# Optimization experiments

Measured on AMD Instinct MI355X. Metric: run time of the kernel, lower is better.

Reference implementation:

```python
import jax, jax.numpy as jnp
import numpy as np
import math

N_HEADS = 16
HEAD_DIM = 64
ROPE_BASE = 10000.0


def _rope_tables(T, head_dim, dtype):
    inv_freq = 1.0 / (ROPE_BASE ** (jnp.arange(0, head_dim, 2, dtype=jnp.float32) / head_dim))
    t = jnp.arange(T, dtype=jnp.float32)
    freqs = jnp.outer(t, inv_freq)          # (T, head_dim/2)
    emb = jnp.concatenate([freqs, freqs], axis=-1)  # (T, head_dim)
    return jnp.cos(emb).astype(dtype), jnp.sin(emb).astype(dtype)


def _rotate_half(x):
    x1, x2 = jnp.split(x, 2, axis=-1)
    return jnp.concatenate([-x2, x1], axis=-1)


def setup_inputs() -> dict:
    key = jax.random.key(0)
    k1, k2, k3 = jax.random.split(key, 3)
    B, T, D = 2, 2048, 1024
    x = jax.random.normal(k1, (B, T, D), dtype=jnp.float32)
    W_qkv = jax.random.normal(k2, (D, 3 * D), dtype=jnp.float32) * (1.0 / math.sqrt(D))
    W_proj = jax.random.normal(k3, (D, D), dtype=jnp.float32) * (1.0 / math.sqrt(D))
    return {"x": x, "W_qkv": W_qkv, "W_proj": W_proj}


def reference(x, W_qkv, W_proj):
    B, T, C = x.shape
    H, Dh = N_HEADS, HEAD_DIM
    qkv = x @ W_qkv                                   # (B,T,3C)
    q, k, v = jnp.split(qkv, 3, axis=-1)
    # (B,T,C) -> (B,H,T,Dh)
    q = q.reshape(B, T, H, Dh).transpose(0, 2, 1, 3)
    k = k.reshape(B, T, H, Dh).transpose(0, 2, 1, 3)
    v = v.reshape(B, T, H, Dh).transpose(0, 2, 1, 3)
    cos, sin = _rope_tables(T, Dh, x.dtype)           # (T,Dh)
    q = q * cos + _rotate_half(q) * sin
    k = k * cos + _rotate_half(k) * sin
    scale = 1.0 / math.sqrt(Dh)
    att = jnp.einsum('bhqd,bhkd->bhqk', q, k) * scale
    causal = jnp.tril(jnp.ones((T, T), dtype=bool))
    att = jnp.where(causal, att, -jnp.inf)
    att = jax.nn.softmax(att, axis=-1)
    y = jnp.einsum('bhqk,bhkd->bhqd', att, v)         # (B,H,T,Dh)
    y = y.transpose(0, 2, 1, 3).reshape(B, T, C)
    return y @ W_proj
```

## Files before the change

kernel.cpp:

```cpp
#include <hip/hip_runtime.h>
#include <hip/hip_bf16.h>
#include <math.h>

typedef __bf16 bf16_t;
typedef __bf16 bf16x8 __attribute__((ext_vector_type(8)));
typedef __bf16 bf16x4 __attribute__((ext_vector_type(4)));
typedef __bf16 bf16x2 __attribute__((ext_vector_type(2)));
typedef float  f32x4  __attribute__((ext_vector_type(4)));
typedef float  f32x16 __attribute__((ext_vector_type(16)));

__device__ __forceinline__ void gload_lds16(const void* g, void* l) {
  __builtin_amdgcn_global_load_lds((const __attribute__((address_space(1))) void*)g,
                                   (__attribute__((address_space(3))) void*)l,
                                   16, 0, 0);
}

__device__ __forceinline__ unsigned pk2(float a, float b) {
  union { bf16x2 h; unsigned u; } x;
  x.h[0] = (bf16_t)a; x.h[1] = (bf16_t)b;
  return x.u;
}
__device__ __forceinline__ bf16x8 frag4(unsigned w0, unsigned w1, unsigned w2, unsigned w3) {
  union { unsigned u[4]; bf16x8 f; } x;
  x.u[0] = w0; x.u[1] = w1; x.u[2] = w2; x.u[3] = w3;
  return x.f;
}
__device__ __forceinline__ void pls(unsigned a, unsigned b, unsigned& x, unsigned& y) {
  auto rr = __builtin_amdgcn_permlane32_swap(a, b, false, false);
  x = ((unsigned*)&rr)[0];
  y = ((unsigned*)&rr)[1];
}

__global__ __launch_bounds__(256) void f32_to_bf16(const float* __restrict__ x,
                                                   bf16_t* __restrict__ y, int n) {
  int i = blockIdx.x * blockDim.x + threadIdx.x;
  int idx = i * 4;
  if (idx < n) {
    float4 v = *(const float4*)(x + idx);
    bf16x4 o;
    o[0] = (bf16_t)v.x; o[1] = (bf16_t)v.y; o[2] = (bf16_t)v.z; o[3] = (bf16_t)v.w;
    *(bf16x4*)(y + idx) = o;
  }
}

__global__ __launch_bounds__(256) void transpose_w(const float* __restrict__ W,
                                                   bf16_t* __restrict__ Wt,
                                                   int K, int N) {
  __shared__ float tile[32][33];
  int tx = threadIdx.x & 31, ty = threadIdx.x >> 5;
  int n0 = blockIdx.x * 32, k0 = blockIdx.y * 32;
  #pragma unroll
  for (int i = 0; i < 4; ++i) {
    int k = ty + i * 8;
    tile[k][tx] = W[(size_t)(k0 + k) * N + n0 + tx];
  }
  __syncthreads();
  #pragma unroll
  for (int i = 0; i < 4; ++i) {
    int r = ty + i * 8;
    Wt[(size_t)(n0 + r) * K + k0 + tx] = (bf16_t)tile[tx][r];
  }
}

__global__ void rope_tables(float* __restrict__ cosT, float* __restrict__ sinT) {
  int t = blockIdx.x, d = threadIdx.x;
  float inv = __expf(-logf(10000.f) * (float)(d & 31) * (1.f / 32.f));
  float ang = (float)t * inv;
  cosT[t * 64 + d] = cosf(ang);
  sinT[t * 64 + d] = sinf(ang);
}

template <int OUT_BF16>
__global__ __launch_bounds__(256) void gemm_bt(const bf16_t* __restrict__ A,
                                               const bf16_t* __restrict__ Bt,
                                               void* __restrict__ Cout,
                                               int M, int N, int K) {
  const int tid = threadIdx.x;
  const int l = tid & 63, w = tid >> 6;
  const int lr = l & 15, lg = l >> 4;
  const int nwgx = gridDim.x, nwgy = gridDim.y;
  const int orig = blockIdx.y * nwgx + blockIdx.x;
  const int cpx = (nwgx * nwgy) >> 3;
  const int s_id = (orig & 7) * cpx + (orig >> 3);
  const int bx = s_id / nwgy;
  const int by = s_id % nwgy;
  const int wr = w >> 1, wc = w & 1;
  __shared__ __align__(16) bf16_t lA[128 * 64];
  __shared__ __align__(16) bf16_t lB[128 * 64];
  f32x4 acc[4][4];
  const f32x4 zf = {0.f, 0.f, 0.f, 0.f};
  #pragma unroll
  for (int m = 0; m < 4; ++m)
    #pragma unroll
    for (int n = 0; n < 4; ++n) acc[m][n] = zf;

  const int sr8 = l >> 3;
  const int sc16 = ((l & 7) * 16) ^ (sr8 << 4);
  const char* Ab = (const char*)(A + (size_t)(by * 128) * K);
  const char* Bb = (const char*)(Bt + (size_t)(bx * 128) * K);
  const size_t rowb = (size_t)K * 2;

  for (int k0 = 0; k0 < 2 * K; k0 += 128) {
    #pragma unroll
    for (int p = 0; p < 4; ++p) {
      int row = p * 32 + w * 8 + sr8;
      gload_lds16(Ab + (size_t)row * rowb + k0 + sc16, (char*)lA + p * 4096 + w * 1024);
      gload_lds16(Bb + (size_t)row * rowb + k0 + sc16, (char*)lB + p * 4096 + w * 1024);
    }
    __syncthreads();
    #pragma unroll
    for (int kk = 0; kk < 2; ++kk) {
      bf16x8 aF[4], bF[4];
      #pragma unroll
      for (int m = 0; m < 4; ++m) {
        int row = wr * 64 + m * 16 + lr;
        aF[m] = *(const bf16x8*)((const char*)lA + row * 128 +
                                 ((kk * 64 + lg * 16) ^ ((row & 7) << 4)));
      }
      #pragma unroll
      for (int n = 0; n < 4; ++n) {
        int row = wc * 64 + n * 16 + lr;
        bF[n] = *(const bf16x8*)((const char*)lB + row * 128 +
                                 ((kk * 64 + lg * 16) ^ ((row & 7) << 4)));
      }
      __builtin_amdgcn_s_setprio(1);
      #pragma unroll
      for (int m = 0; m < 4; ++m)
        #pragma unroll
        for (int n = 0; n < 4; ++n)
          acc[m][n] = __builtin_amdgcn_mfma_f32_16x16x32_bf16(aF[m], bF[n], acc[m][n], 0, 0, 0);
      __builtin_amdgcn_s_setprio(0);
    }
    __syncthreads();
  }

  const int orow0 = by * 128 + wr * 64;
  const int ocol0 = bx * 128 + wc * 64;
  if (OUT_BF16) {
    bf16_t* C = (bf16_t*)Cout;
    #pragma unroll
    for (int m = 0; m < 4; ++m)
      #pragma unroll
      for (int n = 0; n < 4; ++n)
        #pragma unroll
        for (int r = 0; r < 4; ++r)
          C[(size_t)(orow0 + m * 16 + lg * 4 + r) * N + ocol0 + n * 16 + lr] =
              (bf16_t)acc[m][n][r];
  } else {
    float* C = (float*)Cout;
    #pragma unroll
    for (int m = 0; m < 4; ++m)
      #pragma unroll
      for (int n = 0; n < 4; ++n)
        #pragma unroll
        for (int r = 0; r < 4; ++r)
          C[(size_t)(orow0 + m * 16 + lg * 4 + r) * N + ocol0 + n * 16 + lr] =
              acc[m][n][r];
  }
}

__global__ __launch_bounds__(256) void prep_qk(const bf16_t* __restrict__ qkv,
                                               const float* __restrict__ cosT,
                                               const float* __restrict__ sinT,
                                               bf16_t* __restrict__ Q,
                                               bf16_t* __restrict__ Kr) {
  int gid = blockIdx.x * 4 + (threadIdx.x >> 6);
  int d = threadIdx.x & 63;
  int t = gid & 2047, bh = gid >> 11;
  int b = bh >> 4, h = bh & 15;
  const bf16_t* row = qkv + (size_t)(b * 2048 + t) * 3072 + h * 64;
  float q = (float)row[d];
  float k = (float)row[1024 + d];
  float c = cosT[t * 64 + d], s = sinT[t * 64 + d];
  float qp = __shfl_xor(q, 32);
  float kp = __shfl_xor(k, 32);
  float qr = (d < 32) ? -qp : qp;
  float krot = (d < 32) ? -kp : kp;
  size_t o = ((size_t)bh * 2048 + t) * 64 + d;
  Q[o] = (bf16_t)((q * c + qr * s) * 0.18033688011112042f);
  Kr[o] = (bf16_t)(k * c + krot * s);
}

__global__ __launch_bounds__(256) void prep_vt(const bf16_t* __restrict__ qkv,
                                               bf16_t* __restrict__ VT) {
  int bh = blockIdx.x, b = bh >> 4, h = bh & 15;
  int t0 = blockIdx.y * 64;
  __shared__ __align__(16) bf16_t tile[64][72];
  int r = threadIdx.x >> 2, c4 = threadIdx.x & 3;
  const bf16_t* src = qkv + (size_t)(b * 2048 + t0 + r) * 3072 + 2048 + h * 64 + c4 * 16;
  *(bf16x8*)&tile[r][c4 * 16] = *(const bf16x8*)src;
  *(bf16x8*)&tile[r][c4 * 16 + 8] = *(const bf16x8*)(src + 8);
  __syncthreads();
  bf16x8 v0, v1;
  #pragma unroll
  for (int i = 0; i < 8; ++i) v0[i] = tile[c4 * 16 + i][r];
  #pragma unroll
  for (int i = 0; i < 8; ++i) v1[i] = tile[c4 * 16 + 8 + i][r];
  bf16_t* dst = VT + ((size_t)bh * 64 + r) * 2048 + t0 + c4 * 16;
  *(bf16x8*)dst = v0;
  *(bf16x8*)(dst + 8) = v1;
}

__global__ __launch_bounds__(512, 4) void attn(const bf16_t* __restrict__ Q,
                                               const bf16_t* __restrict__ K,
                                               const bf16_t* __restrict__ VT,
                                               bf16_t* __restrict__ Y) {
  const int L = blockIdx.x;
  const int bh = L & 31;
  const int idx = (L & 255) >> 5;
  const int qi = (L >= 256) ? (15 - 2 * idx) : (2 * idx);
  const int b = bh >> 4, h = bh & 15;
  const int tid = threadIdx.x, l = tid & 63, w = tid >> 6;
  const int qw = w & 3, half = w >> 2;
  const int tid2 = tid & 255;
  const int l31 = l & 31, hi = l >> 5;
  const int hi4 = hi * 4, hi8 = hi * 8;
  const int qbase = qi * 128 + qw * 32;
  const int qown = qbase + l31;
  const int ntile = qi + 1;
  const int t0 = half * ntile, tend = t0 + ntile;
  const int tdiag = qbase >> 6;

  __shared__ __align__(16) char smem[65536];
  char* Kbase = smem + half * 16384;
  char* Vbase = smem + 32768 + half * 16384;

  const bf16_t* Qb = Q + (size_t)bh * 2048 * 64;
  const bf16_t* Kb0 = K + (size_t)bh * 2048 * 64;
  const bf16_t* Vb = VT + (size_t)bh * 64 * 2048;

  bf16x8 qf[4];
  #pragma unroll
  for (int kk = 0; kk < 4; ++kk)
    qf[kk] = *(const bf16x8*)(Qb + (size_t)qown * 64 + kk * 16 + hi8);

  const int srow = tid2 >> 3;
  const int scolb = (tid2 & 7) * 16;
  const int rA = srow, rB = 32 + srow;
  const int swA = scolb ^ ((rA & 7) << 4);
  const int swB = scolb ^ ((rB & 7) << 4);
  const char* KgA = (const char*)Kb0 + (size_t)t0 * 8192 + (size_t)rA * 128 + swA;
  const char* KgB = (const char*)Kb0 + (size_t)t0 * 8192 + (size_t)rB * 128 + swB;
  const char* VgA = (const char*)Vb + (size_t)t0 * 128 + (size_t)rA * 4096 + swA;
  const char* VgB = (const char*)Vb + (size_t)t0 * 128 + (size_t)rB * 4096 + swB;

  f32x16 oa[2];
  #pragma unroll
  for (int dt = 0; dt < 2; ++dt)
    #pragma unroll
    for (int r = 0; r < 16; ++r) oa[dt][r] = 0.f;
  float lacc0 = 0.f, lacc1 = 0.f;

  gload_lds16(KgA, Kbase + tid2 * 16);
  gload_lds16(KgB, Kbase + 4096 + tid2 * 16);
  gload_lds16(VgA, Vbase + tid2 * 16);
  gload_lds16(VgB, Vbase + 4096 + tid2 * 16);
  KgA += 8192; KgB += 8192; VgA += 128; VgB += 128;
  __syncthreads();

  int cur = 0;
  for (int t = t0; t < tend; ++t) {
    if (t + 1 < tend) {
      char* dK = Kbase + (cur ^ 1) * 8192;
      char* dV = Vbase + (cur ^ 1) * 8192;
      gload_lds16(KgA, dK + tid2 * 16);
      gload_lds16(KgB, dK + 4096 + tid2 * 16);
      gload_lds16(VgA, dV + tid2 * 16);
      gload_lds16(VgB, dV + 4096 + tid2 * 16);
      KgA += 8192; KgB += 8192; VgA += 128; VgB += 128;
    }
    const char* KlH = Kbase + cur * 8192;
    const char* VlH = Vbase + cur * 8192;

    if (t <= tdiag) {
      f32x16 s[2];
      #pragma unroll
      for (int sb = 0; sb < 2; ++sb)
        #pragma unroll
        for (int r = 0; r < 16; ++r) s[sb][r] = 0.f;
      __builtin_amdgcn_s_setprio(1);
      #pragma unroll
      for (int sb = 0; sb < 2; ++sb) {
        int row = sb * 32 + l31;
        const char* kr = KlH + row * 128;
        int sw = (row & 7) << 4;
        #pragma unroll
        for (int kk = 0; kk < 4; ++kk) {
          bf16x8 kf = *(const bf16x8*)(kr + ((kk * 32 + hi * 16) ^ sw));
          s[sb] = __builtin_amdgcn_mfma_f32_32x32x16_bf16(kf, qf[kk], s[sb], 0, 0, 0);
        }
      }
      __builtin_amdgcn_s_setprio(0);

      if (t == tdiag) {
        #pragma unroll
        for (int sb = 0; sb < 2; ++sb)
          #pragma unroll
          for (int r = 0; r < 16; ++r) {
            int kv = t * 64 + sb * 32 + (r & 3) + 8 * (r >> 2) + hi4;
            if (kv > qown) s[sb][r] = -__builtin_inff();
          }
      }

      #pragma unroll
      for (int r = 0; r < 16; ++r) {
        float p0 = exp2f(s[0][r]);
        float p1 = exp2f(s[1][r]);
        s[0][r] = p0; lacc0 += p0;
        s[1][r] = p1; lacc1 += p1;
      }

      #pragma unroll
      for (int sb = 0; sb < 2; ++sb) {
        unsigned a0 = pk2(s[sb][0], s[sb][1]),   a1 = pk2(s[sb][2], s[sb][3]);
        unsigned b0 = pk2(s[sb][4], s[sb][5]),   b1 = pk2(s[sb][6], s[sb][7]);
        unsigned c0 = pk2(s[sb][8], s[sb][9]),   c1 = pk2(s[sb][10], s[sb][11]);
        unsigned d0 = pk2(s[sb][12], s[sb][13]), d1 = pk2(s[sb][14], s[sb][15]);
        unsigned r0x, r0y, r1x, r1y, r2x, r2y, r3x, r3y;
        pls(a0, b0, r0x, r0y);
        pls(a1, b1, r1x, r1y);
        pls(c0, d0, r2x, r2y);
        pls(c1, d1, r3x, r3y);
        bf16x8 pf0 = frag4(r0x, r1x, r0y, r1y);
        bf16x8 pf1 = frag4(r2x, r3x, r2y, r3y);
        __builtin_amdgcn_s_setprio(1);
        #pragma unroll
        for (int kk = 0; kk < 2; ++kk) {
          bf16x8 pf = kk ? pf1 : pf0;
          #pragma unroll
          for (int dt = 0; dt < 2; ++dt) {
            int vrow = dt * 32 + l31;
            const char* vr = VlH + vrow * 128;
            bf16x8 vf = *(const bf16x8*)(vr + ((sb * 64 + kk * 32 + hi * 16) ^ ((vrow & 7) << 4)));
            oa[dt] = __builtin_amdgcn_mfma_f32_32x32x16_bf16(vf, pf, oa[dt], 0, 0, 0);
          }
        }
        __builtin_amdgcn_s_setprio(0);
      }
    }

    __syncthreads();
    cur ^= 1;
  }

  float lacc = lacc0 + lacc1;
  lacc += __shfl_xor(lacc, 32);
  float* OLDS = (float*)smem;
  float* LLDS = (float*)(smem + 32768);
  if (half == 1) {
    #pragma unroll
    for (int r = 0; r < 32; ++r)
      OLDS[r * 256 + qw * 64 + l] = oa[r >> 4][r & 15];
    LLDS[qw * 64 + l] = lacc;
  }
  __syncthreads();
  if (half == 0) {
    #pragma unroll
    for (int r = 0; r < 32; ++r)
      oa[r >> 4][r & 15] += OLDS[r * 256 + qw * 64 + l];
    float inv = 1.f / (lacc + LLDS[qw * 64 + l]);
    bf16_t* Yb = Y + (size_t)b * 2048 * 1024 + (size_t)qown * 1024 + h * 64;
    #pragma unroll
    for (int dt = 0; dt < 2; ++dt)
      #pragma unroll
      for (int g = 0; g < 4; ++g) {
        bf16x4 v;
        #pragma unroll
        for (int jj = 0; jj < 4; ++jj) v[jj] = (bf16_t)(oa[dt][g * 4 + jj] * inv);
        *(bf16x4*)(Yb + dt * 32 + g * 8 + hi4) = v;
      }
  }
}

extern "C" void kernel_launch(void* const* d_in, const int* in_sizes, int n_in,
                              void* d_out, int out_size, void* d_ws, size_t ws_size,
                              hipStream_t stream) {
  const float* x = (const float*)d_in[0];
  const float* Wqkv = (const float*)d_in[1];
  const float* Wproj = (const float*)d_in[2];
  float* out = (float*)d_out;
  char* ws = (char*)d_ws;

  bf16_t* xb     = (bf16_t*)(ws + (0u));
  bf16_t* wqkvt  = (bf16_t*)(ws + (8u << 20));
  bf16_t* wprojt = (bf16_t*)(ws + (14u << 20));
  bf16_t* qkv    = (bf16_t*)(ws + (16u << 20));
  bf16_t* Q      = (bf16_t*)(ws + (40u << 20));
  bf16_t* Kr     = (bf16_t*)(ws + (48u << 20));
  bf16_t* VT     = (bf16_t*)(ws + (56u << 20));
  bf16_t* Y      = (bf16_t*)(ws + (64u << 20));
  float*  cosT   = (float*)(ws + (72u << 20));
  float*  sinT   = (float*)(ws + (72u << 20) + (1u << 19));

  f32_to_bf16<<<dim3(4096), dim3(256), 0, stream>>>(x, xb, 4096 * 1024);
  transpose_w<<<dim3(96, 32), dim3(256), 0, stream>>>(Wqkv, wqkvt, 1024, 3072);
  transpose_w<<<dim3(32, 32), dim3(256), 0, stream>>>(Wproj, wprojt, 1024, 1024);
  rope_tables<<<dim3(2048), dim3(64), 0, stream>>>(cosT, sinT);
  gemm_bt<1><<<dim3(24, 32), dim3(256), 0, stream>>>(xb, wqkvt, (void*)qkv, 4096, 3072, 1024);
  prep_qk<<<dim3(16384), dim3(256), 0, stream>>>(qkv, cosT, sinT, Q, Kr);
  prep_vt<<<dim3(32, 32), dim3(256), 0, stream>>>(qkv, VT);
  attn<<<dim3(512), dim3(512), 0, stream>>>(Q, Kr, VT, Y);
  gemm_bt<0><<<dim3(8, 32), dim3(256), 0, stream>>>(Y, wprojt, (void*)out, 4096, 1024, 1024);
}
```

Baseline: 122.6 us.

## Merge prep kernels into fewer launches and split attention PV accumulators

```diff
diff --git a/kernel.cpp b/kernel.cpp
--- a/kernel.cpp
+++ b/kernel.cpp
@@ -31,43 +31,52 @@
   y = ((unsigned*)&rr)[1];
 }
 
-__global__ __launch_bounds__(256) void f32_to_bf16(const float* __restrict__ x,
-                                                   bf16_t* __restrict__ y, int n) {
-  int i = blockIdx.x * blockDim.x + threadIdx.x;
-  int idx = i * 4;
-  if (idx < n) {
+__global__ __launch_bounds__(256) void prep_all(const float* __restrict__ x,
+                                                const float* __restrict__ Wqkv,
+                                                const float* __restrict__ Wproj,
+                                                bf16_t* __restrict__ xb,
+                                                bf16_t* __restrict__ wqkvt,
+                                                bf16_t* __restrict__ wprojt,
+                                                float* __restrict__ cosT,
+                                                float* __restrict__ sinT) {
+  __shared__ float tile[32][33];
+  int bx = blockIdx.x;
+  if (bx < 4096) {
+    int idx = (bx * 256 + threadIdx.x) * 4;
     float4 v = *(const float4*)(x + idx);
     bf16x4 o;
     o[0] = (bf16_t)v.x; o[1] = (bf16_t)v.y; o[2] = (bf16_t)v.z; o[3] = (bf16_t)v.w;
-    *(bf16x4*)(y + idx) = o;
-  }
-}
-
-__global__ __launch_bounds__(256) void transpose_w(const float* __restrict__ W,
-                                                   bf16_t* __restrict__ Wt,
-                                                   int K, int N) {
-  __shared__ float tile[32][33];
-  int tx = threadIdx.x & 31, ty = threadIdx.x >> 5;
-  int n0 = blockIdx.x * 32, k0 = blockIdx.y * 32;
-  #pragma unroll
-  for (int i = 0; i < 4; ++i) {
-    int k = ty + i * 8;
-    tile[k][tx] = W[(size_t)(k0 + k) * N + n0 + tx];
-  }
-  __syncthreads();
-  #pragma unroll
-  for (int i = 0; i < 4; ++i) {
-    int r = ty + i * 8;
-    Wt[(size_t)(n0 + r) * K + k0 + tx] = (bf16_t)tile[tx][r];
-  }
-}
-
-__global__ void rope_tables(float* __restrict__ cosT, float* __restrict__ sinT) {
-  int t = blockIdx.x, d = threadIdx.x;
-  float inv = __expf(-logf(10000.f) * (float)(d & 31) * (1.f / 32.f));
-  float ang = (float)t * inv;
-  cosT[t * 64 + d] = cosf(ang);
-  sinT[t * 64 + d] = sinf(ang);
+    *(bf16x4*)(xb + idx) = o;
+  } else if (bx < 8192) {
+    const float* W; bf16_t* Wt; int K, N, n0, k0;
+    if (bx < 7168) {
+      W = Wqkv; Wt = wqkvt; K = 1024; N = 3072;
+      int b = bx - 4096; n0 = (b % 96) * 32; k0 = (b / 96) * 32;
+    } else {
+      W = Wproj; Wt = wprojt; K = 1024; N = 1024;
+      int b = bx - 7168; n0 = (b & 31) * 32; k0 = (b >> 5) * 32;
+    }
+    int tx = threadIdx.x & 31, ty = threadIdx.x >> 5;
+    #pragma unroll
+    for (int i = 0; i < 4; ++i) {
+      int k = ty + i * 8;
+      tile[k][tx] = W[(size_t)(k0 + k) * N + n0 + tx];
+    }
+    __syncthreads();
+    #pragma unroll
+    for (int i = 0; i < 4; ++i) {
+      int r = ty + i * 8;
+      Wt[(size_t)(n0 + r) * K + k0 + tx] = (bf16_t)tile[tx][r];
+    }
+  } else {
+    int b = bx - 8192;
+    int t = b * 4 + (threadIdx.x >> 6);
+    int d = threadIdx.x & 63;
+    float inv = __expf(-logf(10000.f) * (float)(d & 31) * (1.f / 32.f));
+    float ang = (float)t * inv;
+    cosT[t * 64 + d] = cosf(ang);
+    sinT[t * 64 + d] = sinf(ang);
+  }
 }
 
 template <int OUT_BF16>
@@ -123,13 +132,11 @@
         bF[n] = *(const bf16x8*)((const char*)lB + row * 128 +
                                  ((kk * 64 + lg * 16) ^ ((row & 7) << 4)));
       }
-      __builtin_amdgcn_s_setprio(1);
       #pragma unroll
       for (int m = 0; m < 4; ++m)
         #pragma unroll
         for (int n = 0; n < 4; ++n)
           acc[m][n] = __builtin_amdgcn_mfma_f32_16x16x32_bf16(aF[m], bF[n], acc[m][n], 0, 0, 0);
-      __builtin_amdgcn_s_setprio(0);
     }
     __syncthreads();
   }
@@ -159,46 +166,48 @@
   }
 }
 
-__global__ __launch_bounds__(256) void prep_qk(const bf16_t* __restrict__ qkv,
-                                               const float* __restrict__ cosT,
-                                               const float* __restrict__ sinT,
-                                               bf16_t* __restrict__ Q,
-                                               bf16_t* __restrict__ Kr) {
-  int gid = blockIdx.x * 4 + (threadIdx.x >> 6);
-  int d = threadIdx.x & 63;
-  int t = gid & 2047, bh = gid >> 11;
-  int b = bh >> 4, h = bh & 15;
-  const bf16_t* row = qkv + (size_t)(b * 2048 + t) * 3072 + h * 64;
-  float q = (float)row[d];
-  float k = (float)row[1024 + d];
-  float c = cosT[t * 64 + d], s = sinT[t * 64 + d];
-  float qp = __shfl_xor(q, 32);
-  float kp = __shfl_xor(k, 32);
-  float qr = (d < 32) ? -qp : qp;
-  float krot = (d < 32) ? -kp : kp;
-  size_t o = ((size_t)bh * 2048 + t) * 64 + d;
-  Q[o] = (bf16_t)((q * c + qr * s) * 0.18033688011112042f);
-  Kr[o] = (bf16_t)(k * c + krot * s);
-}
-
-__global__ __launch_bounds__(256) void prep_vt(const bf16_t* __restrict__ qkv,
-                                               bf16_t* __restrict__ VT) {
-  int bh = blockIdx.x, b = bh >> 4, h = bh & 15;
-  int t0 = blockIdx.y * 64;
+__global__ __launch_bounds__(256) void prep_qkv(const bf16_t* __restrict__ qkv,
+                                                const float* __restrict__ cosT,
+                                                const float* __restrict__ sinT,
+                                                bf16_t* __restrict__ Q,
+                                                bf16_t* __restrict__ Kr,
+                                                bf16_t* __restrict__ VT) {
   __shared__ __align__(16) bf16_t tile[64][72];
-  int r = threadIdx.x >> 2, c4 = threadIdx.x & 3;
-  const bf16_t* src = qkv + (size_t)(b * 2048 + t0 + r) * 3072 + 2048 + h * 64 + c4 * 16;
-  *(bf16x8*)&tile[r][c4 * 16] = *(const bf16x8*)src;
-  *(bf16x8*)&tile[r][c4 * 16 + 8] = *(const bf16x8*)(src + 8);
-  __syncthreads();
-  bf16x8 v0, v1;
-  #pragma unroll
-  for (int i = 0; i < 8; ++i) v0[i] = tile[c4 * 16 + i][r];
-  #pragma unroll
-  for (int i = 0; i < 8; ++i) v1[i] = tile[c4 * 16 + 8 + i][r];
-  bf16_t* dst = VT + ((size_t)bh * 64 + r) * 2048 + t0 + c4 * 16;
-  *(bf16x8*)dst = v0;
-  *(bf16x8*)(dst + 8) = v1;
+  int bx = blockIdx.x;
+  if (bx < 16384) {
+    int gid = bx * 4 + (threadIdx.x >> 6);
+    int d = threadIdx.x & 63;
+    int t = gid & 2047, bh = gid >> 11;
+    int b = bh >> 4, h = bh & 15;
+    const bf16_t* row = qkv + (size_t)(b * 2048 + t) * 3072 + h * 64;
+    float q = (float)row[d];
+    float k = (float)row[1024 + d];
+    float c = cosT[t * 64 + d], s = sinT[t * 64 + d];
+    float qp = __shfl_xor(q, 32);
+    float kp = __shfl_xor(k, 32);
+    float qr = (d < 32) ? -qp : qp;
+    float krot = (d < 32) ? -kp : kp;
+    size_t o = ((size_t)bh * 2048 + t) * 64 + d;
+    Q[o] = (bf16_t)((q * c + qr * s) * 0.18033688011112042f);
+    Kr[o] = (bf16_t)(k * c + krot * s);
+  } else {
+    int b2 = bx - 16384;
+    int bh = b2 & 31, b = bh >> 4, h = bh & 15;
+    int t0 = (b2 >> 5) * 64;
+    int r = threadIdx.x >> 2, c4 = threadIdx.x & 3;
+    const bf16_t* src = qkv + (size_t)(b * 2048 + t0 + r) * 3072 + 2048 + h * 64 + c4 * 16;
+    *(bf16x8*)&tile[r][c4 * 16] = *(const bf16x8*)src;
+    *(bf16x8*)&tile[r][c4 * 16 + 8] = *(const bf16x8*)(src + 8);
+    __syncthreads();
+    bf16x8 v0, v1;
+    #pragma unroll
+    for (int i = 0; i < 8; ++i) v0[i] = tile[c4 * 16 + i][r];
+    #pragma unroll
+    for (int i = 0; i < 8; ++i) v1[i] = tile[c4 * 16 + 8 + i][r];
+    bf16_t* dst = VT + ((size_t)bh * 64 + r) * 2048 + t0 + c4 * 16;
+    *(bf16x8*)dst = v0;
+    *(bf16x8*)(dst + 8) = v1;
+  }
 }
 
 __global__ __launch_bounds__(512, 4) void attn(const bf16_t* __restrict__ Q,
@@ -244,11 +253,14 @@
   const char* VgA = (const char*)Vb + (size_t)t0 * 128 + (size_t)rA * 4096 + swA;
   const char* VgB = (const char*)Vb + (size_t)t0 * 128 + (size_t)rB * 4096 + swB;
 
-  f32x16 oa[2];
+  f32x16 Z;
   #pragma unroll
-  for (int dt = 0; dt < 2; ++dt)
-    #pragma unroll
-    for (int r = 0; r < 16; ++r) oa[dt][r] = 0.f;
+  for (int r = 0; r < 16; ++r) Z[r] = 0.f;
+  f32x16 oacc[2][2];
+  #pragma unroll
+  for (int sb = 0; sb < 2; ++sb)
+    #pragma unroll
+    for (int dt = 0; dt < 2; ++dt) oacc[sb][dt] = Z;
   float lacc0 = 0.f, lacc1 = 0.f;
 
   gload_lds16(KgA, Kbase + tid2 * 16);
@@ -275,22 +287,18 @@
     if (t <= tdiag) {
       f32x16 s[2];
       #pragma unroll
-      for (int sb = 0; sb < 2; ++sb)
-        #pragma unroll
-        for (int r = 0; r < 16; ++r) s[sb][r] = 0.f;
-      __builtin_amdgcn_s_setprio(1);
-      #pragma unroll
       for (int sb = 0; sb < 2; ++sb) {
         int row = sb * 32 + l31;
         const char* kr = KlH + row * 128;
         int sw = (row & 7) << 4;
-        #pragma unroll
-        for (int kk = 0; kk < 4; ++kk) {
+        bf16x8 kf0 = *(const bf16x8*)(kr + ((hi * 16) ^ sw));
+        s[sb] = __builtin_amdgcn_mfma_f32_32x32x16_bf16(kf0, qf[0], Z, 0, 0, 0);
+        #pragma unroll
+        for (int kk = 1; kk < 4; ++kk) {
           bf16x8 kf = *(const bf16x8*)(kr + ((kk * 32 + hi * 16) ^ sw));
           s[sb] = __builtin_amdgcn_mfma_f32_32x32x16_bf16(kf, qf[kk], s[sb], 0, 0, 0);
         }
       }
-      __builtin_amdgcn_s_setprio(0);
 
       if (t == tdiag) {
         #pragma unroll
@@ -323,7 +331,6 @@
         pls(c1, d1, r3x, r3y);
         bf16x8 pf0 = frag4(r0x, r1x, r0y, r1y);
         bf16x8 pf1 = frag4(r2x, r3x, r2y, r3y);
-        __builtin_amdgcn_s_setprio(1);
         #pragma unroll
         for (int kk = 0; kk < 2; ++kk) {
           bf16x8 pf = kk ? pf1 : pf0;
@@ -332,10 +339,9 @@
             int vrow = dt * 32 + l31;
             const char* vr = VlH + vrow * 128;
             bf16x8 vf = *(const bf16x8*)(vr + ((sb * 64 + kk * 32 + hi * 16) ^ ((vrow & 7) << 4)));
-            oa[dt] = __builtin_amdgcn_mfma_f32_32x32x16_bf16(vf, pf, oa[dt], 0, 0, 0);
+            oacc[sb][dt] = __builtin_amdgcn_mfma_f32_32x32x16_bf16(vf, pf, oacc[sb][dt], 0, 0, 0);
           }
         }
-        __builtin_amdgcn_s_setprio(0);
       }
     }
 
@@ -343,6 +349,9 @@
     cur ^= 1;
   }
 
+  f32x16 oa2[2];
+  oa2[0] = oacc[0][0] + oacc[1][0];
+  oa2[1] = oacc[0][1] + oacc[1][1];
   float lacc = lacc0 + lacc1;
   lacc += __shfl_xor(lacc, 32);
   float* OLDS = (float*)smem;
@@ -350,14 +359,14 @@
   if (half == 1) {
     #pragma unroll
     for (int r = 0; r < 32; ++r)
-      OLDS[r * 256 + qw * 64 + l] = oa[r >> 4][r & 15];
+      OLDS[r * 256 + qw * 64 + l] = oa2[r >> 4][r & 15];
     LLDS[qw * 64 + l] = lacc;
   }
   __syncthreads();
   if (half == 0) {
     #pragma unroll
     for (int r = 0; r < 32; ++r)
-      oa[r >> 4][r & 15] += OLDS[r * 256 + qw * 64 + l];
+      oa2[r >> 4][r & 15] += OLDS[r * 256 + qw * 64 + l];
     float inv = 1.f / (lacc + LLDS[qw * 64 + l]);
     bf16_t* Yb = Y + (size_t)b * 2048 * 1024 + (size_t)qown * 1024 + h * 64;
     #pragma unroll
@@ -366,7 +375,7 @@
       for (int g = 0; g < 4; ++g) {
         bf16x4 v;
         #pragma unroll
-        for (int jj = 0; jj < 4; ++jj) v[jj] = (bf16_t)(oa[dt][g * 4 + jj] * inv);
+        for (int jj = 0; jj < 4; ++jj) v[jj] = (bf16_t)(oa2[dt][g * 4 + jj] * inv);
         *(bf16x4*)(Yb + dt * 32 + g * 8 + hi4) = v;
       }
   }
@@ -392,13 +401,9 @@
   float*  cosT   = (float*)(ws + (72u << 20));
   float*  sinT   = (float*)(ws + (72u << 20) + (1u << 19));
 
-  f32_to_bf16<<<dim3(4096), dim3(256), 0, stream>>>(x, xb, 4096 * 1024);
-  transpose_w<<<dim3(96, 32), dim3(256), 0, stream>>>(Wqkv, wqkvt, 1024, 3072);
-  transpose_w<<<dim3(32, 32), dim3(256), 0, stream>>>(Wproj, wprojt, 1024, 1024);
-  rope_tables<<<dim3(2048), dim3(64), 0, stream>>>(cosT, sinT);
+  prep_all<<<dim3(8704), dim3(256), 0, stream>>>(x, Wqkv, Wproj, xb, wqkvt, wprojt, cosT, sinT);
   gemm_bt<1><<<dim3(24, 32), dim3(256), 0, stream>>>(xb, wqkvt, (void*)qkv, 4096, 3072, 1024);
-  prep_qk<<<dim3(16384), dim3(256), 0, stream>>>(qkv, cosT, sinT, Q, Kr);
-  prep_vt<<<dim3(32, 32), dim3(256), 0, stream>>>(qkv, VT);
+  prep_qkv<<<dim3(17408), dim3(256), 0, stream>>>(qkv, cosT, sinT, Q, Kr, VT);
   attn<<<dim3(512), dim3(512), 0, stream>>>(Q, Kr, VT, Y);
   gemm_bt<0><<<dim3(8, 32), dim3(256), 0, stream>>>(Y, wprojt, (void*)out, 4096, 1024, 1024);
 }
```

New measurement: 156.8 us. +27.9%, slower.
